# Kernel optimization log

Measured on AMD Instinct MI355X. Metric: run time of the kernel, lower is better.

Reference implementation:

```python
import jax, jax.numpy as jnp
import numpy as np

NUM_CLASSES = 2
NORM_EPS = 1e-12   # F.normalize default
COS_EPS = 1e-8     # nn.CosineSimilarity default
MEAN_EPS = 1e-6


def _l2_normalize_c(x):
    # normalize over channel dim (dim=1), per (batch, pixel) -- matches
    # F.normalize(x.view(-1,16,256*256), dim=1)
    n = jnp.sqrt(jnp.sum(x * x, axis=1, keepdims=True))
    return x / jnp.maximum(n, NORM_EPS)


def _cos_c(a, b):
    # cosine similarity along channel dim, torch semantics
    dot = jnp.sum(a * b, axis=1)
    na = jnp.sqrt(jnp.sum(a * a, axis=1))
    nb = jnp.sqrt(jnp.sum(b * b, axis=1))
    return dot / jnp.maximum(na * nb, COS_EPS)


def setup_inputs() -> dict:
    key = jax.random.key(0)
    k1, k2, k3 = jax.random.split(key, 3)
    preds_S = jax.random.normal(k1, (32, 16, 256, 256), dtype=jnp.float32)
    preds_T = jax.random.normal(k2, (32, 16, 256, 256), dtype=jnp.float32)
    target = jax.random.randint(k3, (32, 256, 256), 0, NUM_CLASSES, dtype=jnp.int64)
    return {"preds_S": preds_S, "preds_T": preds_T, "target": target}


def reference(preds_S, preds_T, target):
    feat_S = _l2_normalize_c(preds_S)  # [B,16,H,W]
    feat_T = _l2_normalize_c(preds_T)
    # target is already HxW == feature size, so nearest upsample is identity
    tar = target[:, None, :, :].astype(feat_S.dtype)  # [B,1,H,W], broadcasts over C

    center_S, center_T = feat_S, feat_T
    center_S_FS, center_T_FS = feat_S, feat_T
    for i in range(NUM_CLASSES):
        mask = (tar == i).astype(feat_S.dtype)  # [B,1,H,W]
        cnt = jnp.sum(mask, axis=(-2, -1)) + MEAN_EPS  # [B,1]
        mean_S = (jnp.sum(mask * feat_S, axis=(-2, -1)) / cnt)[:, :, None, None]  # [B,16,1,1]
        mean_T = (jnp.sum(mask * feat_T, axis=(-2, -1)) / cnt)[:, :, None, None]
        center_S = (1.0 - mask) * center_S + mask * mean_S
        center_T = (1.0 - mask) * center_T + mask * mean_T
        center_S_FS = mask * center_S_FS + (1.0 - mask) * mean_S
        center_T_FS = mask * center_T_FS + (1.0 - mask) * mean_T

    pcsim_S = jnp.exp(_cos_c(feat_S, center_S) - _cos_c(feat_S, center_S_FS))
    pcsim_T = jnp.exp(_cos_c(feat_T, center_T) - _cos_c(feat_T, center_T_FS))
    return jnp.mean((pcsim_S - pcsim_T) ** 2)
```

## Files before the change

kernel.cpp:

```cpp
#include <hip/hip_runtime.h>
#include <math.h>

#define NBATCH 32
#define NCH 16
#define HW 65536
#define SLICES1 32
#define SLICES2 32
#define TPB 256

#define WS_SUMS_S 0
#define WS_SUMS_T 1024
#define WS_N1     2048
#define WS_LOSS   2080
#define WS_FLOATS 2112

__device__ __forceinline__ float wave_sum(float v) {
#pragma unroll
  for (int off = 32; off > 0; off >>= 1) v += __shfl_down(v, off, 64);
  return v;
}

__global__ __launch_bounds__(TPB) void k_sums(const float* __restrict__ S,
                                              const float* __restrict__ T,
                                              const int* __restrict__ tgt,
                                              float* __restrict__ ws) {
  const int b = blockIdx.y;
  const int slice = blockIdx.x;
  const int which = blockIdx.z;
  const int tid = threadIdx.x;
  const int wid = tid >> 6;

  const float* Xb = (which ? T : S) + (size_t)b * NCH * HW;
  const int* tb = tgt + (size_t)b * HW;
  float* dst = ws + (which ? WS_SUMS_T : WS_SUMS_S) + b * 32;

  const int off = (wid + ((slice & 3) << 2) + b + (which << 3)) & 15;

  const int base = slice * (HW / SLICES1) + tid * 4;

  float acc0[NCH], acc1[NCH];
#pragma unroll
  for (int i = 0; i < NCH; ++i) { acc0[i] = 0.f; acc1[i] = 0.f; }
  float n1 = 0.f;

  for (int it = 0; it < 2; ++it) {
    const int p = base + it * (TPB * 4);
    const int4 tv = *(const int4*)(tb + p);
    float4 x[NCH];
#pragma unroll
    for (int i = 0; i < NCH; ++i) {
      const int cc = (i + off) & 15;
      x[i] = *(const float4*)(Xb + (size_t)cc * HW + p);
    }

    const float m0 = (tv.x == 1) ? 1.f : 0.f;
    const float m1 = (tv.y == 1) ? 1.f : 0.f;
    const float m2 = (tv.z == 1) ? 1.f : 0.f;
    const float m3 = (tv.w == 1) ? 1.f : 0.f;
    n1 += (m0 + m1) + (m2 + m3);

    float s0a = 0.f, s0b = 0.f, s1a = 0.f, s1b = 0.f;
    float s2a = 0.f, s2b = 0.f, s3a = 0.f, s3b = 0.f;
#pragma unroll
    for (int i = 0; i < NCH; i += 2) {
      s0a = fmaf(x[i].x, x[i].x, s0a);   s0b = fmaf(x[i + 1].x, x[i + 1].x, s0b);
      s1a = fmaf(x[i].y, x[i].y, s1a);   s1b = fmaf(x[i + 1].y, x[i + 1].y, s1b);
      s2a = fmaf(x[i].z, x[i].z, s2a);   s2b = fmaf(x[i + 1].z, x[i + 1].z, s2b);
      s3a = fmaf(x[i].w, x[i].w, s3a);   s3b = fmaf(x[i + 1].w, x[i + 1].w, s3b);
    }
    const float i0 = 1.f / fmaxf(sqrtf(s0a + s0b), 1e-12f);
    const float i1 = 1.f / fmaxf(sqrtf(s1a + s1b), 1e-12f);
    const float i2 = 1.f / fmaxf(sqrtf(s2a + s2b), 1e-12f);
    const float i3 = 1.f / fmaxf(sqrtf(s3a + s3b), 1e-12f);

#pragma unroll
    for (int i = 0; i < NCH; ++i) {
      const float f0 = x[i].x * i0, f1 = x[i].y * i1;
      const float f2 = x[i].z * i2, f3 = x[i].w * i3;
      const float t_ = (f0 + f1) + (f2 + f3);
      const float m_ = fmaf(f0, m0, fmaf(f1, m1, fmaf(f2, m2, f3 * m3)));
      acc1[i] += m_;
      acc0[i] += t_ - m_;
    }
  }

  __shared__ float lds[32][TPB + 1];
  __shared__ float redn[4];
#pragma unroll
  for (int i = 0; i < NCH; ++i) {
    const int r = (i + off) & 15;
    lds[r][tid] = acc0[i];
    lds[16 + r][tid] = acc1[i];
  }
  n1 = wave_sum(n1);
  if ((tid & 63) == 0) redn[wid] = n1;
  __syncthreads();

  const int row = tid >> 3, seg = tid & 7;
  float s = 0.f;
#pragma unroll
  for (int k0 = 0; k0 < 32; ++k0) {
    const int k = (k0 + seg * 4) & 31;
    s += lds[row][seg * 32 + k];
  }
  s += __shfl_down(s, 4, 8);
  s += __shfl_down(s, 2, 8);
  s += __shfl_down(s, 1, 8);
  if (seg == 0) atomicAdd(dst + row, s);
  if (tid == 0 && which == 0)
    atomicAdd(ws + WS_N1 + b, redn[0] + redn[1] + redn[2] + redn[3]);
}

__device__ __forceinline__ float pc_one(float ss, float d0, float d1, int t,
                                        float nm0, float nm1) {
  const float n = sqrtf(ss);
  const float inv = 1.f / fmaxf(n, 1e-12f);
  const float na = n * inv;
  const float c0 = (d0 * inv) / fmaxf(na * nm0, 1e-8f);
  const float c1 = (d1 * inv) / fmaxf(na * nm1, 1e-8f);
  return expf((t == 1) ? (c1 - c0) : (c0 - c1));
}

__global__ __launch_bounds__(TPB) void k_pass2(const float* __restrict__ S,
                                               const float* __restrict__ T,
                                               const int* __restrict__ tgt,
                                               float* __restrict__ ws) {
  __shared__ __align__(16) float sm[72];
  __shared__ float red[4];
  const int b = blockIdx.y;
  const int slice = blockIdx.x;
  const int tid = threadIdx.x;
  const int wid = tid >> 6;

  const int offS = (wid + ((slice & 3) << 2) + b) & 15;
  const int offT = (offS + 8) & 15;

  const int base = slice * (HW / SLICES2) + tid * 2;
  const float* Sb = S + (size_t)b * NCH * HW;
  const float* Tb = T + (size_t)b * NCH * HW;
  const int* tb = tgt + (size_t)b * HW;

  if (tid < 64) {
    const int t = tid >> 5, cls = (tid >> 4) & 1, ch = tid & 15;
    const float n1v = ws[WS_N1 + b];
    const float cnt = (cls ? n1v : ((float)HW - n1v)) + 1e-6f;
    const float s = ws[(t ? WS_SUMS_T : WS_SUMS_S) + b * 32 + cls * 16 + ch];
    sm[tid] = s / cnt;
  }
  __syncthreads();
  if (tid < 4) {
    float ss = 0.f;
    const int base_ = (tid >> 1) * 32 + (tid & 1) * 16;
#pragma unroll
    for (int c = 0; c < NCH; ++c) { const float v = sm[base_ + c]; ss = fmaf(v, v, ss); }
    sm[64 + tid] = sqrtf(ss);
  }
  __syncthreads();

  const float nmS0 = sm[64], nmS1 = sm[65], nmT0 = sm[66], nmT1 = sm[67];
  float lacc = 0.f;

  for (int it = 0; it < 4; ++it) {
    const int p = base + it * (TPB * 2);
    const int2 tv = *(const int2*)(tb + p);
    float2 xs[NCH], xt[NCH];
#pragma unroll
    for (int i = 0; i < NCH; ++i)
      xs[i] = *(const float2*)(Sb + (size_t)((i + offS) & 15) * HW + p);
#pragma unroll
    for (int i = 0; i < NCH; ++i)
      xt[i] = *(const float2*)(Tb + (size_t)((i + offT) & 15) * HW + p);

    float ss0 = 0.f, ss1 = 0.f, d00 = 0.f, d01 = 0.f, d10 = 0.f, d11 = 0.f;
#pragma unroll
    for (int i = 0; i < NCH; ++i) {
      const int cc = (i + offS) & 15;
      const float w0 = sm[cc], w1 = sm[16 + cc];
      ss0 = fmaf(xs[i].x, xs[i].x, ss0); ss1 = fmaf(xs[i].y, xs[i].y, ss1);
      d00 = fmaf(xs[i].x, w0, d00);      d01 = fmaf(xs[i].y, w0, d01);
      d10 = fmaf(xs[i].x, w1, d10);      d11 = fmaf(xs[i].y, w1, d11);
    }
    const float pcS0 = pc_one(ss0, d00, d10, tv.x, nmS0, nmS1);
    const float pcS1 = pc_one(ss1, d01, d11, tv.y, nmS0, nmS1);

    ss0 = 0.f; ss1 = 0.f; d00 = 0.f; d01 = 0.f; d10 = 0.f; d11 = 0.f;
#pragma unroll
    for (int i = 0; i < NCH; ++i) {
      const int cc = (i + offT) & 15;
      const float w0 = sm[32 + cc], w1 = sm[48 + cc];
      ss0 = fmaf(xt[i].x, xt[i].x, ss0); ss1 = fmaf(xt[i].y, xt[i].y, ss1);
      d00 = fmaf(xt[i].x, w0, d00);      d01 = fmaf(xt[i].y, w0, d01);
      d10 = fmaf(xt[i].x, w1, d10);      d11 = fmaf(xt[i].y, w1, d11);
    }
    const float pcT0 = pc_one(ss0, d00, d10, tv.x, nmT0, nmT1);
    const float pcT1 = pc_one(ss1, d01, d11, tv.y, nmT0, nmT1);

    const float e0 = pcS0 - pcT0, e1 = pcS1 - pcT1;
    lacc += e0 * e0 + e1 * e1;
  }

  lacc = wave_sum(lacc);
  if ((tid & 63) == 0) red[tid >> 6] = lacc;
  __syncthreads();
  if (tid == 0)
    atomicAdd(ws + WS_LOSS + b, red[0] + red[1] + red[2] + red[3]);
}

__global__ void k_final(const float* __restrict__ ws, float* __restrict__ out) {
  const int lane = threadIdx.x & 63;
  float v = (lane < NBATCH) ? ws[WS_LOSS + lane] : 0.f;
  v = wave_sum(v);
  if (lane == 0) out[0] = v * (1.f / 2097152.f);
}

extern "C" void kernel_launch(void* const* d_in, const int* in_sizes, int n_in,
                              void* d_out, int out_size, void* d_ws, size_t ws_size,
                              hipStream_t stream) {
  const float* S = (const float*)d_in[0];
  const float* T = (const float*)d_in[1];
  const int* tgt = (const int*)d_in[2];
  float* ws = (float*)d_ws;
  float* out = (float*)d_out;

  hipMemsetAsync(d_ws, 0, WS_FLOATS * sizeof(float), stream);
  dim3 g1(SLICES1, NBATCH, 2);
  k_sums<<<g1, TPB, 0, stream>>>(S, T, tgt, ws);
  dim3 g2(SLICES2, NBATCH);
  k_pass2<<<g2, TPB, 0, stream>>>(S, T, tgt, ws);
  k_final<<<1, 64, 0, stream>>>(ws, out);
}
```

Measured before the change: 335.1 us.

## Stage k_sums tiles through LDS via async global_load_lds and use nontemporal loads

k_sums now uses twice as many slices, each handling a single 1024-pixel tile. All 16 channels of the tile are copied into a 64 KB shared buffer with global_load_lds async copies and then read back as float4, replacing direct strided global loads. The same buffer is reused afterwards for the cross-thread reduction. k_pass2 switches its S/T loads to nontemporal loads to avoid polluting cache. The large LDS footprint limits occupancy, and the extra slices double the number of atomics per batch.

```diff
diff --git a/kernel.cpp b/kernel.cpp
--- a/kernel.cpp
+++ b/kernel.cpp
@@ -4,7 +4,7 @@
 #define NBATCH 32
 #define NCH 16
 #define HW 65536
-#define SLICES1 32
+#define SLICES1 64
 #define SLICES2 32
 #define TPB 256
 
@@ -14,86 +14,96 @@
 #define WS_LOSS   2080
 #define WS_FLOATS 2112
 
+typedef float v2f __attribute__((ext_vector_type(2)));
+
 __device__ __forceinline__ float wave_sum(float v) {
 #pragma unroll
   for (int off = 32; off > 0; off >>= 1) v += __shfl_down(v, off, 64);
   return v;
+}
+
+__device__ __forceinline__ void async_copy16(const float* g, float* l) {
+  __builtin_amdgcn_global_load_lds(
+      (const __attribute__((address_space(1))) void*)g,
+      (__attribute__((address_space(3))) void*)l, 16, 0, 0);
 }
 
 __global__ __launch_bounds__(TPB) void k_sums(const float* __restrict__ S,
                                               const float* __restrict__ T,
                                               const int* __restrict__ tgt,
                                               float* __restrict__ ws) {
+  __shared__ __align__(16) float smem[16 * 1024];
   const int b = blockIdx.y;
   const int slice = blockIdx.x;
   const int which = blockIdx.z;
   const int tid = threadIdx.x;
-  const int wid = tid >> 6;
+  const int lane = tid & 63, wid = tid >> 6;
 
   const float* Xb = (which ? T : S) + (size_t)b * NCH * HW;
   const int* tb = tgt + (size_t)b * HW;
   float* dst = ws + (which ? WS_SUMS_T : WS_SUMS_S) + b * 32;
 
-  const int off = (wid + ((slice & 3) << 2) + b + (which << 3)) & 15;
-
-  const int base = slice * (HW / SLICES1) + tid * 4;
+  const int tilebase = slice * 1024;
+
+  const int4 tv = *(const int4*)(tb + tilebase + tid * 4);
+#pragma unroll
+  for (int j = 0; j < 4; ++j) {
+    const int r = (wid << 2) + j;
+#pragma unroll
+    for (int k = 0; k < 4; ++k) {
+      const int chunk = (k + j) & 3;
+      async_copy16(Xb + (size_t)r * HW + tilebase + chunk * 256 + lane * 4,
+                   &smem[r * 1024 + chunk * 256]);
+    }
+  }
+  __syncthreads();
+
+  float4 x[NCH];
+#pragma unroll
+  for (int c = 0; c < NCH; ++c) x[c] = *(const float4*)&smem[c * 1024 + tid * 4];
+
+  const float m0 = (tv.x == 1) ? 1.f : 0.f;
+  const float m1 = (tv.y == 1) ? 1.f : 0.f;
+  const float m2 = (tv.z == 1) ? 1.f : 0.f;
+  const float m3 = (tv.w == 1) ? 1.f : 0.f;
+  float n1 = (m0 + m1) + (m2 + m3);
+
+  float s0a = 0.f, s0b = 0.f, s1a = 0.f, s1b = 0.f;
+  float s2a = 0.f, s2b = 0.f, s3a = 0.f, s3b = 0.f;
+#pragma unroll
+  for (int i = 0; i < NCH; i += 2) {
+    s0a = fmaf(x[i].x, x[i].x, s0a);   s0b = fmaf(x[i + 1].x, x[i + 1].x, s0b);
+    s1a = fmaf(x[i].y, x[i].y, s1a);   s1b = fmaf(x[i + 1].y, x[i + 1].y, s1b);
+    s2a = fmaf(x[i].z, x[i].z, s2a);   s2b = fmaf(x[i + 1].z, x[i + 1].z, s2b);
+    s3a = fmaf(x[i].w, x[i].w, s3a);   s3b = fmaf(x[i + 1].w, x[i + 1].w, s3b);
+  }
+  const float i0 = 1.f / fmaxf(sqrtf(s0a + s0b), 1e-12f);
+  const float i1 = 1.f / fmaxf(sqrtf(s1a + s1b), 1e-12f);
+  const float i2 = 1.f / fmaxf(sqrtf(s2a + s2b), 1e-12f);
+  const float i3 = 1.f / fmaxf(sqrtf(s3a + s3b), 1e-12f);
 
   float acc0[NCH], acc1[NCH];
 #pragma unroll
-  for (int i = 0; i < NCH; ++i) { acc0[i] = 0.f; acc1[i] = 0.f; }
-  float n1 = 0.f;
-
-  for (int it = 0; it < 2; ++it) {
-    const int p = base + it * (TPB * 4);
-    const int4 tv = *(const int4*)(tb + p);
-    float4 x[NCH];
-#pragma unroll
-    for (int i = 0; i < NCH; ++i) {
-      const int cc = (i + off) & 15;
-      x[i] = *(const float4*)(Xb + (size_t)cc * HW + p);
-    }
-
-    const float m0 = (tv.x == 1) ? 1.f : 0.f;
-    const float m1 = (tv.y == 1) ? 1.f : 0.f;
-    const float m2 = (tv.z == 1) ? 1.f : 0.f;
-    const float m3 = (tv.w == 1) ? 1.f : 0.f;
-    n1 += (m0 + m1) + (m2 + m3);
-
-    float s0a = 0.f, s0b = 0.f, s1a = 0.f, s1b = 0.f;
-    float s2a = 0.f, s2b = 0.f, s3a = 0.f, s3b = 0.f;
-#pragma unroll
-    for (int i = 0; i < NCH; i += 2) {
-      s0a = fmaf(x[i].x, x[i].x, s0a);   s0b = fmaf(x[i + 1].x, x[i + 1].x, s0b);
-      s1a = fmaf(x[i].y, x[i].y, s1a);   s1b = fmaf(x[i + 1].y, x[i + 1].y, s1b);
-      s2a = fmaf(x[i].z, x[i].z, s2a);   s2b = fmaf(x[i + 1].z, x[i + 1].z, s2b);
-      s3a = fmaf(x[i].w, x[i].w, s3a);   s3b = fmaf(x[i + 1].w, x[i + 1].w, s3b);
-    }
-    const float i0 = 1.f / fmaxf(sqrtf(s0a + s0b), 1e-12f);
-    const float i1 = 1.f / fmaxf(sqrtf(s1a + s1b), 1e-12f);
-    const float i2 = 1.f / fmaxf(sqrtf(s2a + s2b), 1e-12f);
-    const float i3 = 1.f / fmaxf(sqrtf(s3a + s3b), 1e-12f);
-
-#pragma unroll
-    for (int i = 0; i < NCH; ++i) {
-      const float f0 = x[i].x * i0, f1 = x[i].y * i1;
-      const float f2 = x[i].z * i2, f3 = x[i].w * i3;
-      const float t_ = (f0 + f1) + (f2 + f3);
-      const float m_ = fmaf(f0, m0, fmaf(f1, m1, fmaf(f2, m2, f3 * m3)));
-      acc1[i] += m_;
-      acc0[i] += t_ - m_;
-    }
-  }
-
-  __shared__ float lds[32][TPB + 1];
-  __shared__ float redn[4];
-#pragma unroll
   for (int i = 0; i < NCH; ++i) {
-    const int r = (i + off) & 15;
-    lds[r][tid] = acc0[i];
-    lds[16 + r][tid] = acc1[i];
+    const float f0 = x[i].x * i0, f1 = x[i].y * i1;
+    const float f2 = x[i].z * i2, f3 = x[i].w * i3;
+    const float t_ = (f0 + f1) + (f2 + f3);
+    const float m_ = fmaf(f0, m0, fmaf(f1, m1, fmaf(f2, m2, f3 * m3)));
+    acc1[i] = m_;
+    acc0[i] = t_ - m_;
   }
   n1 = wave_sum(n1);
-  if ((tid & 63) == 0) redn[wid] = n1;
+
+  __syncthreads();
+
+  float (*red)[257] = (float(*)[257])smem;
+  float* redn = smem + 16000;
+#pragma unroll
+  for (int i = 0; i < NCH; ++i) {
+    red[i][tid] = acc0[i];
+    red[16 + i][tid] = acc1[i];
+  }
+  if (lane == 0) redn[wid] = n1;
   __syncthreads();
 
   const int row = tid >> 3, seg = tid & 7;
@@ -101,7 +111,7 @@
 #pragma unroll
   for (int k0 = 0; k0 < 32; ++k0) {
     const int k = (k0 + seg * 4) & 31;
-    s += lds[row][seg * 32 + k];
+    s += red[row][seg * 32 + k];
   }
   s += __shfl_down(s, 4, 8);
   s += __shfl_down(s, 2, 8);
@@ -163,13 +173,15 @@
   for (int it = 0; it < 4; ++it) {
     const int p = base + it * (TPB * 2);
     const int2 tv = *(const int2*)(tb + p);
-    float2 xs[NCH], xt[NCH];
+    v2f xs[NCH], xt[NCH];
 #pragma unroll
     for (int i = 0; i < NCH; ++i)
-      xs[i] = *(const float2*)(Sb + (size_t)((i + offS) & 15) * HW + p);
+      xs[i] = __builtin_nontemporal_load(
+          (const v2f*)(Sb + (size_t)((i + offS) & 15) * HW + p));
 #pragma unroll
     for (int i = 0; i < NCH; ++i)
-      xt[i] = *(const float2*)(Tb + (size_t)((i + offT) & 15) * HW + p);
+      xt[i] = __builtin_nontemporal_load(
+          (const v2f*)(Tb + (size_t)((i + offT) & 15) * HW + p));
 
     float ss0 = 0.f, ss1 = 0.f, d00 = 0.f, d01 = 0.f, d10 = 0.f, d11 = 0.f;
 #pragma unroll
```

Result: faster. 326.5 us (-2.6%).

## Replace atomics and memset with per-block partials and last-block final reduction

Applied to the files above, without the earlier changes.

Removes the workspace memset and the separate final kernel. k_sums now writes per-slice partial sums instead of using atomics, and k_pass2 reduces those partials itself. k_pass2 also finishes the loss with a last-block-done counter. The channel-rotation offsets that staggered memory access are dropped, which may bring back channel or bank conflicts. Each k_pass2 block now redundantly re-reduces 32 slice partials, adding a small amount of extra work per block.

```diff
diff --git a/kernel.cpp b/kernel.cpp
--- a/kernel.cpp
+++ b/kernel.cpp
@@ -7,12 +7,13 @@
 #define SLICES1 32
 #define SLICES2 32
 #define TPB 256
-
-#define WS_SUMS_S 0
-#define WS_SUMS_T 1024
-#define WS_N1     2048
-#define WS_LOSS   2080
-#define WS_FLOATS 2112
+#define NBLK2 (SLICES2 * NBATCH)
+
+#define WS_PART  0
+#define WS_N1P   65536
+#define WS_LOSSP 66560
+#define WS_CNT   67584
+#define WS_FLOATS 67600
 
 __device__ __forceinline__ float wave_sum(float v) {
 #pragma unroll
@@ -28,13 +29,13 @@
   const int slice = blockIdx.x;
   const int which = blockIdx.z;
   const int tid = threadIdx.x;
-  const int wid = tid >> 6;
+  const int lane = tid & 63, wid = tid >> 6;
+
+  if (slice == 0 && b == 0 && which == 0 && tid == 0)
+    *reinterpret_cast<int*>(ws + WS_CNT) = 0;
 
   const float* Xb = (which ? T : S) + (size_t)b * NCH * HW;
   const int* tb = tgt + (size_t)b * HW;
-  float* dst = ws + (which ? WS_SUMS_T : WS_SUMS_S) + b * 32;
-
-  const int off = (wid + ((slice & 3) << 2) + b + (which << 3)) & 15;
 
   const int base = slice * (HW / SLICES1) + tid * 4;
 
@@ -48,10 +49,8 @@
     const int4 tv = *(const int4*)(tb + p);
     float4 x[NCH];
 #pragma unroll
-    for (int i = 0; i < NCH; ++i) {
-      const int cc = (i + off) & 15;
-      x[i] = *(const float4*)(Xb + (size_t)cc * HW + p);
-    }
+    for (int i = 0; i < NCH; ++i)
+      x[i] = *(const float4*)(Xb + (size_t)i * HW + p);
 
     const float m0 = (tv.x == 1) ? 1.f : 0.f;
     const float m1 = (tv.y == 1) ? 1.f : 0.f;
@@ -88,12 +87,11 @@
   __shared__ float redn[4];
 #pragma unroll
   for (int i = 0; i < NCH; ++i) {
-    const int r = (i + off) & 15;
-    lds[r][tid] = acc0[i];
-    lds[16 + r][tid] = acc1[i];
+    lds[i][tid] = acc0[i];
+    lds[16 + i][tid] = acc1[i];
   }
   n1 = wave_sum(n1);
-  if ((tid & 63) == 0) redn[wid] = n1;
+  if (lane == 0) redn[wid] = n1;
   __syncthreads();
 
   const int row = tid >> 3, seg = tid & 7;
@@ -106,9 +104,11 @@
   s += __shfl_down(s, 4, 8);
   s += __shfl_down(s, 2, 8);
   s += __shfl_down(s, 1, 8);
-  if (seg == 0) atomicAdd(dst + row, s);
+
+  float* part = ws + WS_PART + (((size_t)which * NBATCH + b) * SLICES1 + slice) * 32;
+  if (seg == 0) part[row] = s;
   if (tid == 0 && which == 0)
-    atomicAdd(ws + WS_N1 + b, redn[0] + redn[1] + redn[2] + redn[3]);
+    ws[WS_N1P + b * SLICES1 + slice] = redn[0] + redn[1] + redn[2] + redn[3];
 }
 
 __device__ __forceinline__ float pc_one(float ss, float d0, float d1, int t,
@@ -124,39 +124,52 @@
 __global__ __launch_bounds__(TPB) void k_pass2(const float* __restrict__ S,
                                                const float* __restrict__ T,
                                                const int* __restrict__ tgt,
-                                               float* __restrict__ ws) {
+                                               float* __restrict__ ws,
+                                               float* __restrict__ out) {
   __shared__ __align__(16) float sm[72];
-  __shared__ float red[4];
+  __shared__ float ldp[4][64];
+  __shared__ float ldn[32];
+  __shared__ float red4[4];
+  __shared__ int isLast;
   const int b = blockIdx.y;
   const int slice = blockIdx.x;
   const int tid = threadIdx.x;
-  const int wid = tid >> 6;
-
-  const int offS = (wid + ((slice & 3) << 2) + b) & 15;
-  const int offT = (offS + 8) & 15;
+
+  {
+    const int c64 = tid & 63, q = tid >> 6;
+    const int t_ = c64 >> 5, c32 = c64 & 31;
+    const float* pp = ws + WS_PART + (((size_t)t_ * NBATCH + b) * SLICES1) * 32 + c32;
+    float s8 = 0.f;
+#pragma unroll
+    for (int k = 0; k < 8; ++k) s8 += pp[(q * 8 + k) * 32];
+    ldp[q][c64] = s8;
+  }
+  if (tid < 32) ldn[tid] = ws[WS_N1P + b * SLICES1 + tid];
+  __syncthreads();
+
+  if (tid < 64) {
+    float n1 = 0.f;
+#pragma unroll
+    for (int k = 0; k < 32; ++k) n1 += ldn[k];
+    const int cls = (tid >> 4) & 1;
+    const float cnt = (cls ? n1 : ((float)HW - n1)) + 1e-6f;
+    sm[tid] = (ldp[0][tid] + ldp[1][tid] + ldp[2][tid] + ldp[3][tid]) / cnt;
+  }
+  __syncthreads();
+  if (tid < 4) {
+    float ss = 0.f;
+    const int base_ = (tid >> 1) * 32 + (tid & 1) * 16;
+#pragma unroll
+    for (int c = 0; c < NCH; ++c) { const float v = sm[base_ + c]; ss = fmaf(v, v, ss); }
+    sm[64 + tid] = sqrtf(ss);
+  }
+  __syncthreads();
 
   const int base = slice * (HW / SLICES2) + tid * 2;
   const float* Sb = S + (size_t)b * NCH * HW;
   const float* Tb = T + (size_t)b * NCH * HW;
   const int* tb = tgt + (size_t)b * HW;
 
-  if (tid < 64) {
-    const int t = tid >> 5, cls = (tid >> 4) & 1, ch = tid & 15;
-    const float n1v = ws[WS_N1 + b];
-    const float cnt = (cls ? n1v : ((float)HW - n1v)) + 1e-6f;
-    const float s = ws[(t ? WS_SUMS_T : WS_SUMS_S) + b * 32 + cls * 16 + ch];
-    sm[tid] = s / cnt;
-  }
-  __syncthreads();
-  if (tid < 4) {
-    float ss = 0.f;
-    const int base_ = (tid >> 1) * 32 + (tid & 1) * 16;
-#pragma unroll
-    for (int c = 0; c < NCH; ++c) { const float v = sm[base_ + c]; ss = fmaf(v, v, ss); }
-    sm[64 + tid] = sqrtf(ss);
-  }
-  __syncthreads();
-
   const float nmS0 = sm[64], nmS1 = sm[65], nmT0 = sm[66], nmT1 = sm[67];
   float lacc = 0.f;
 
@@ -166,16 +179,15 @@
     float2 xs[NCH], xt[NCH];
 #pragma unroll
     for (int i = 0; i < NCH; ++i)
-      xs[i] = *(const float2*)(Sb + (size_t)((i + offS) & 15) * HW + p);
+      xs[i] = *(const float2*)(Sb + (size_t)i * HW + p);
 #pragma unroll
     for (int i = 0; i < NCH; ++i)
-      xt[i] = *(const float2*)(Tb + (size_t)((i + offT) & 15) * HW + p);
+      xt[i] = *(const float2*)(Tb + (size_t)i * HW + p);
 
     float ss0 = 0.f, ss1 = 0.f, d00 = 0.f, d01 = 0.f, d10 = 0.f, d11 = 0.f;
 #pragma unroll
     for (int i = 0; i < NCH; ++i) {
-      const int cc = (i + offS) & 15;
-      const float w0 = sm[cc], w1 = sm[16 + cc];
+      const float w0 = sm[i], w1 = sm[16 + i];
       ss0 = fmaf(xs[i].x, xs[i].x, ss0); ss1 = fmaf(xs[i].y, xs[i].y, ss1);
       d00 = fmaf(xs[i].x, w0, d00);      d01 = fmaf(xs[i].y, w0, d01);
       d10 = fmaf(xs[i].x, w1, d10);      d11 = fmaf(xs[i].y, w1, d11);
@@ -186,8 +198,7 @@
     ss0 = 0.f; ss1 = 0.f; d00 = 0.f; d01 = 0.f; d10 = 0.f; d11 = 0.f;
 #pragma unroll
     for (int i = 0; i < NCH; ++i) {
-      const int cc = (i + offT) & 15;
-      const float w0 = sm[32 + cc], w1 = sm[48 + cc];
+      const float w0 = sm[32 + i], w1 = sm[48 + i];
       ss0 = fmaf(xt[i].x, xt[i].x, ss0); ss1 = fmaf(xt[i].y, xt[i].y, ss1);
       d00 = fmaf(xt[i].x, w0, d00);      d01 = fmaf(xt[i].y, w0, d01);
       d10 = fmaf(xt[i].x, w1, d10);      d11 = fmaf(xt[i].y, w1, d11);
@@ -200,17 +211,28 @@
   }
 
   lacc = wave_sum(lacc);
-  if ((tid & 63) == 0) red[tid >> 6] = lacc;
-  __syncthreads();
-  if (tid == 0)
-    atomicAdd(ws + WS_LOSS + b, red[0] + red[1] + red[2] + red[3]);
-}
-
-__global__ void k_final(const float* __restrict__ ws, float* __restrict__ out) {
-  const int lane = threadIdx.x & 63;
-  float v = (lane < NBATCH) ? ws[WS_LOSS + lane] : 0.f;
-  v = wave_sum(v);
-  if (lane == 0) out[0] = v * (1.f / 2097152.f);
+  if ((tid & 63) == 0) red4[tid >> 6] = lacc;
+  __syncthreads();
+
+  const int bidx = b * SLICES2 + slice;
+  if (tid == 0) {
+    ws[WS_LOSSP + bidx] = red4[0] + red4[1] + red4[2] + red4[3];
+    __threadfence();
+    const int old = atomicAdd(reinterpret_cast<int*>(ws + WS_CNT), 1);
+    isLast = (old == NBLK2 - 1);
+  }
+  __syncthreads();
+
+  if (isLast) {
+    __threadfence();
+    if (tid < 64) {
+      float s = 0.f;
+#pragma unroll
+      for (int k = 0; k < NBLK2 / 64; ++k) s += ws[WS_LOSSP + tid + 64 * k];
+      s = wave_sum(s);
+      if (tid == 0) out[0] = s * (1.f / 2097152.f);
+    }
+  }
 }
 
 extern "C" void kernel_launch(void* const* d_in, const int* in_sizes, int n_in,
@@ -222,10 +244,8 @@
   float* ws = (float*)d_ws;
   float* out = (float*)d_out;
 
-  hipMemsetAsync(d_ws, 0, WS_FLOATS * sizeof(float), stream);
   dim3 g1(SLICES1, NBATCH, 2);
   k_sums<<<g1, TPB, 0, stream>>>(S, T, tgt, ws);
   dim3 g2(SLICES2, NBATCH);
-  k_pass2<<<g2, TPB, 0, stream>>>(S, T, tgt, ws);
-  k_final<<<1, 64, 0, stream>>>(ws, out);
-}
+  k_pass2<<<g2, TPB, 0, stream>>>(S, T, tgt, ws, out);
+}
```

After: 364.6 us. 8.8% more time.
